# Performance work log

Measured on AMD Instinct MI355X. Metric: run time of the kernel, lower is better.

The kernel has to match this reference:

```python
import jax, jax.numpy as jnp
import numpy as np


def setup_inputs() -> dict:
    key = jax.random.key(0)
    ks = jax.random.split(key, 8)
    B, N, A, H = 2, 2048, 256, 8
    KD = A // H  # key_dim per head = 32
    VD = A // H  # value_dim per head = 32
    return {
        "q_data": jax.random.normal(ks[0], (B, N, A), dtype=jnp.float32),
        "bias": jax.random.normal(ks[1], (B, N), dtype=jnp.float32),
        "nonbatched_bias": jax.random.normal(ks[2], (H, N, N), dtype=jnp.float32),
        "query_w": jax.random.normal(ks[3], (A, H, KD), dtype=jnp.float32) * 0.05,
        "query_b": jax.random.normal(ks[4], (1, H, KD), dtype=jnp.float32) * 0.05,
        "key_w": jax.random.normal(ks[5], (A, H, KD), dtype=jnp.float32) * 0.05,
        "value_w": jax.random.normal(ks[6], (A, H, VD), dtype=jnp.float32) * 0.05,
        "gating_w": jax.random.normal(ks[7], (A, H, VD), dtype=jnp.float32) * 0.05,
    }


def reference(q_data, bias, nonbatched_bias, query_w, query_b, key_w, value_w, gating_w):
    # q_data: [b, n, a]; bias: [b, n_k]; nonbatched_bias: [h, n_q, n_k]
    key_dim = query_w.shape[-1]
    scale = key_dim ** (-0.5)
    # projections (fused QKV in the original kernel)
    q = (jnp.einsum("bqa,ahc->bqhc", q_data, query_w) + query_b) * scale  # [b,q,h,c]
    k = jnp.einsum("bka,ahc->bkhc", q_data, key_w)                        # [b,k,h,c]
    v = jnp.einsum("bka,ahv->bkhv", q_data, value_w)                      # [b,k,h,v]
    # attention logits + batched bias (over keys) + shared nonbatched bias
    logits = jnp.einsum("bqhc,bkhc->bhqk", q, k)
    logits = logits + bias[:, None, None, :] + nonbatched_bias[None]
    weights = jax.nn.softmax(logits, axis=-1)                             # [b,h,q,k]
    weighted = jnp.einsum("bhqk,bkhv->bqhv", weights, v)                  # [b,q,h,v]
    # sigmoid gating branch fused after value projection
    gate = jax.nn.sigmoid(jnp.einsum("bqa,ahv->bqhv", q_data, gating_w))
    return weighted * gate                                                # [b,q,h,v]
```

## Files before the change

### kernel.cpp

```cpp
#include <hip/hip_runtime.h>
#include <stdint.h>

#define NTOK 2048
#define SCALE 0.17677669529663687f
#define SM_SHIFT 24.0f

typedef short s16x8 __attribute__((ext_vector_type(8)));
typedef unsigned short u16x8 __attribute__((ext_vector_type(8)));
typedef float f32x4 __attribute__((ext_vector_type(4)));

__device__ __forceinline__ unsigned short f2bf(float f) {
  unsigned int u = __builtin_bit_cast(unsigned int, f);
  u += 0x7fffu + ((u >> 16) & 1u);
  return (unsigned short)(u >> 16);
}

__device__ __forceinline__ void gld_lds16(const float* g, float* l) {
  __builtin_amdgcn_global_load_lds(
      (const __attribute__((address_space(1))) unsigned int*)g,
      (__attribute__((address_space(3))) unsigned int*)l, 16, 0, 0);
}

__global__ __launch_bounds__(256) void prep_weights_k(
    const float* __restrict__ qw, const float* __restrict__ kw,
    const float* __restrict__ vw, const float* __restrict__ gw,
    unsigned short* __restrict__ Wt) {
  __shared__ float tile[64][68];
  const int p = blockIdx.z;
  const int a0 = blockIdx.x * 64;
  const int n0 = blockIdx.y * 64;
  const float* src = (p == 0) ? qw : (p == 1) ? kw : (p == 2) ? vw : gw;
  const int tx = threadIdx.x & 15;
  const int ty = threadIdx.x >> 4;
#pragma unroll
  for (int kk = 0; kk < 4; kk++) {
    int ar = ty + kk * 16;
    float4 v = *reinterpret_cast<const float4*>(src + (a0 + ar) * 256 + n0 + tx * 4);
    tile[ar][tx * 4 + 0] = v.x; tile[ar][tx * 4 + 1] = v.y;
    tile[ar][tx * 4 + 2] = v.z; tile[ar][tx * 4 + 3] = v.w;
  }
  __syncthreads();
  unsigned short* dst = Wt + p * 65536;
#pragma unroll
  for (int kk = 0; kk < 4; kk++) {
    int nr = ty + kk * 16;
    ushort4 o;
    o.x = f2bf(tile[tx * 4 + 0][nr]);
    o.y = f2bf(tile[tx * 4 + 1][nr]);
    o.z = f2bf(tile[tx * 4 + 2][nr]);
    o.w = f2bf(tile[tx * 4 + 3][nr]);
    *reinterpret_cast<ushort4*>(dst + (n0 + nr) * 256 + a0 + tx * 4) = o;
  }
}

__global__ __launch_bounds__(256) void proj_k(
    const float* __restrict__ x, const unsigned short* __restrict__ Wt,
    const float* __restrict__ query_b,
    unsigned short* __restrict__ Qg, unsigned short* __restrict__ Kg,
    unsigned short* __restrict__ Vt, float* __restrict__ gate) {
  const int w = threadIdx.x >> 6;
  const int lane = threadIdx.x & 63;
  const int l15 = lane & 15;
  const int quad = lane >> 4;
  const int p = blockIdx.y >> 1;
  const int half = blockIdx.y & 1;
  const int rbase = blockIdx.x * 128 + w * 32;
  const unsigned short* wp = Wt + p * 65536;

  f32x4 acc[2][8];
#pragma unroll
  for (int rt = 0; rt < 2; rt++)
#pragma unroll
    for (int ct = 0; ct < 8; ct++) acc[rt][ct] = (f32x4){0.f, 0.f, 0.f, 0.f};

  for (int ks = 0; ks < 8; ks++) {
    const int kb = ks * 32;
    s16x8 af[2];
#pragma unroll
    for (int rt = 0; rt < 2; rt++) {
      const float* xr = x + (rbase + rt * 16 + l15) * 256 + kb + quad * 8;
      float4 f0 = *reinterpret_cast<const float4*>(xr);
      float4 f1 = *reinterpret_cast<const float4*>(xr + 4);
      u16x8 t;
      t[0] = f2bf(f0.x); t[1] = f2bf(f0.y); t[2] = f2bf(f0.z); t[3] = f2bf(f0.w);
      t[4] = f2bf(f1.x); t[5] = f2bf(f1.y); t[6] = f2bf(f1.z); t[7] = f2bf(f1.w);
      af[rt] = __builtin_bit_cast(s16x8, t);
    }
#pragma unroll
    for (int ct = 0; ct < 8; ct++) {
      uint4 bv = *reinterpret_cast<const uint4*>(
          wp + (half * 128 + ct * 16 + l15) * 256 + kb + quad * 8);
      s16x8 bfr = __builtin_bit_cast(s16x8, bv);
#pragma unroll
      for (int rt = 0; rt < 2; rt++)
        acc[rt][ct] = __builtin_amdgcn_mfma_f32_16x16x32_bf16(af[rt], bfr, acc[rt][ct], 0, 0, 0);
    }
  }

#pragma unroll
  for (int ct = 0; ct < 8; ct++) {
    const int cgl = half * 128 + ct * 16 + l15;
    const int h = cgl >> 5, c = cgl & 31;
#pragma unroll
    for (int rt = 0; rt < 2; rt++) {
      const int n0r = rbase + rt * 16 + quad * 4;
      const int bidx = n0r >> 11;
      const int nl0 = n0r & 2047;
      if (p == 0) {
        const float qb = query_b[cgl];
#pragma unroll
        for (int i = 0; i < 4; i++) {
          float v = (acc[rt][ct][i] + qb) * SCALE;
          Qg[(size_t)((bidx * 8 + h) * 2048 + nl0 + i) * 32 + c] = f2bf(v);
        }
      } else if (p == 1) {
#pragma unroll
        for (int i = 0; i < 4; i++)
          Kg[(size_t)((bidx * 8 + h) * 2048 + nl0 + i) * 32 + c] = f2bf(acc[rt][ct][i]);
      } else if (p == 2) {
        ushort4 o;
        o.x = f2bf(acc[rt][ct][0]); o.y = f2bf(acc[rt][ct][1]);
        o.z = f2bf(acc[rt][ct][2]); o.w = f2bf(acc[rt][ct][3]);
        *reinterpret_cast<ushort4*>(Vt + (size_t)((bidx * 8 + h) * 32 + c) * 2048 + nl0) = o;
      } else {
#pragma unroll
        for (int i = 0; i < 4; i++) {
          float s = 1.f / (1.f + __expf(-acc[rt][ct][i]));
          gate[(size_t)(bidx * 2048 + nl0 + i) * 256 + cgl] = s;
        }
      }
    }
  }
}

#define PST 72
__global__ __launch_bounds__(256, 4) void attn_k(
    const unsigned short* __restrict__ Qg, const unsigned short* __restrict__ Kg,
    const unsigned short* __restrict__ Vt, const float* __restrict__ bias,
    const float* __restrict__ nb,
    float* __restrict__ po, float* __restrict__ pl) {
  __shared__ float NbS[2][32 * 64];
  __shared__ unsigned short Ps[4 * 16 * PST];
  const int w = threadIdx.x >> 6;
  const int lane = threadIdx.x & 63;
  const int l15 = lane & 15;
  const int quad = lane >> 4;
  const int qsub = w >> 1;
  const int b = w & 1;
  const int h = blockIdx.y;
  const int sp = blockIdx.z;
  const int bh = b * 8 + h;
  const int qtile = blockIdx.x * 32;
  const int qbase = qtile + qsub * 16;
  const int kt0 = sp * 16;
  const unsigned short* Qp = Qg + (size_t)bh * 2048 * 32;
  const unsigned short* Kp = Kg + (size_t)bh * 2048 * 32;
  const unsigned short* Vp = Vt + (size_t)bh * 32 * 2048;
  const float* biasp = bias + b * 2048;
  unsigned short* Pw = Ps + w * 16 * PST;

  const float* nbl[2];
  {
    const float* nbt = nb + (size_t)h * 2048 * 2048 + (size_t)qtile * 2048;
#pragma unroll
    for (int j = 0; j < 2; j++) {
      const int r = w * 8 + j * 4 + (lane >> 4);
      const int cblk = (lane & 15) ^ (r & 7);
      nbl[j] = nbt + (size_t)r * 2048 + cblk * 4;
    }
  }

  s16x8 aq = __builtin_bit_cast(s16x8, *reinterpret_cast<const uint4*>(
      Qp + (size_t)(qbase + l15) * 32 + quad * 8));
  const int qr0 = qbase + quad * 4;

  int nbrow[4], nbkey[4];
#pragma unroll
  for (int i = 0; i < 4; i++) {
    const int rl = qsub * 16 + quad * 4 + i;
    nbrow[i] = rl * 64;
    nbkey[i] = rl & 7;
  }

  float lst[4];
  f32x4 o[2];
#pragma unroll
  for (int i = 0; i < 4; i++) lst[i] = 0.f;
#pragma unroll
  for (int vt = 0; vt < 2; vt++) o[vt] = (f32x4){0.f, 0.f, 0.f, 0.f};

  float bb[4];
#pragma unroll
  for (int ct = 0; ct < 4; ct++) bb[ct] = biasp[kt0 * 64 + ct * 16 + l15];

#pragma unroll
  for (int j = 0; j < 2; j++)
    gld_lds16(nbl[j] + kt0 * 64, &NbS[0][(w * 8 + j * 4) * 64]);
  __syncthreads();

#pragma unroll 2
  for (int kt = kt0; kt < kt0 + 16; kt++) {
    const int kb = kt * 64;
    const int cur = kt & 1, nxt = cur ^ 1;

    s16x8 bk[4];
#pragma unroll
    for (int ct = 0; ct < 4; ct++)
      bk[ct] = __builtin_bit_cast(s16x8, *reinterpret_cast<const uint4*>(
          Kp + (size_t)(kb + ct * 16 + l15) * 32 + quad * 8));

    s16x8 vbf[2][2];
#pragma unroll
    for (int kc = 0; kc < 2; kc++)
#pragma unroll
      for (int vt = 0; vt < 2; vt++)
        vbf[kc][vt] = __builtin_bit_cast(s16x8, *reinterpret_cast<const uint4*>(
            Vp + (size_t)(vt * 16 + l15) * 2048 + kb + kc * 32 + quad * 8));

    if (kt < kt0 + 15) {
#pragma unroll
      for (int j = 0; j < 2; j++)
        gld_lds16(nbl[j] + (kb + 64), &NbS[nxt][(w * 8 + j * 4) * 64]);
    }

    f32x4 s[4];
#pragma unroll
    for (int ct = 0; ct < 4; ct++) {
#pragma unroll
      for (int i = 0; i < 4; i++) {
        const int slot = ((ct * 4 + (l15 >> 2)) ^ nbkey[i]) * 4 + (l15 & 3);
        s[ct][i] = bb[ct] + NbS[cur][nbrow[i] + slot];
      }
    }

#pragma unroll
    for (int ct = 0; ct < 4; ct++)
      s[ct] = __builtin_amdgcn_mfma_f32_16x16x32_bf16(aq, bk[ct], s[ct], 0, 0, 0);

    if (kt < kt0 + 15) {
      const int kb2 = kb + 64;
#pragma unroll
      for (int ct = 0; ct < 4; ct++) bb[ct] = biasp[kb2 + ct * 16 + l15];
    }

#pragma unroll
    for (int i = 0; i < 4; i++) {
      float sum = 0.f;
#pragma unroll
      for (int ct = 0; ct < 4; ct++) {
        float pv = __expf(s[ct][i] - SM_SHIFT);
        Pw[(quad * 4 + i) * PST + ct * 16 + l15] = f2bf(pv);
        sum += pv;
      }
      lst[i] += sum;
    }

#pragma unroll
    for (int kc = 0; kc < 2; kc++) {
      s16x8 ap = __builtin_bit_cast(s16x8, *reinterpret_cast<const uint4*>(
          &Pw[l15 * PST + kc * 32 + quad * 8]));
#pragma unroll
      for (int vt = 0; vt < 2; vt++)
        o[vt] = __builtin_amdgcn_mfma_f32_16x16x32_bf16(ap, vbf[kc][vt], o[vt], 0, 0, 0);
    }

    __syncthreads();
  }

  const size_t pbase = (size_t)(sp * 16 + bh) * 2048;
#pragma unroll
  for (int vt = 0; vt < 2; vt++)
#pragma unroll
    for (int i = 0; i < 4; i++)
      po[(pbase + qr0 + i) * 32 + vt * 16 + l15] = o[vt][i];
#pragma unroll
  for (int i = 0; i < 4; i++) {
    lst[i] += __shfl_xor(lst[i], 1);
    lst[i] += __shfl_xor(lst[i], 2);
    lst[i] += __shfl_xor(lst[i], 4);
    lst[i] += __shfl_xor(lst[i], 8);
  }
  if (l15 == 0) {
#pragma unroll
    for (int i = 0; i < 4; i++) pl[pbase + qr0 + i] = lst[i];
  }
}

__global__ __launch_bounds__(256) void combine_k(
    const float* __restrict__ po, const float* __restrict__ pl,
    const float* __restrict__ gate, float* __restrict__ out) {
  const int bq = blockIdx.x;
  const int b = bq >> 11, q = bq & 2047;
  const int h = threadIdx.x >> 5, v = threadIdx.x & 31;
  const int bh = b * 8 + h;
  const size_t i0 = (size_t)(0 * 16 + bh) * 2048 + q;
  const size_t i1 = (size_t)(1 * 16 + bh) * 2048 + q;
  const float l = pl[i0] + pl[i1];
  const float ov = po[i0 * 32 + v] + po[i1 * 32 + v];
  const size_t oidx = (size_t)(b * 2048 + q) * 256 + h * 32 + v;
  out[oidx] = (ov / l) * gate[oidx];
}

extern "C" void kernel_launch(void* const* d_in, const int* in_sizes, int n_in,
                              void* d_out, int out_size, void* d_ws, size_t ws_size,
                              hipStream_t stream) {
  const float* q_data = (const float*)d_in[0];
  const float* bias = (const float*)d_in[1];
  const float* nbb = (const float*)d_in[2];
  const float* qw = (const float*)d_in[3];
  const float* qb = (const float*)d_in[4];
  const float* kw = (const float*)d_in[5];
  const float* vw = (const float*)d_in[6];
  const float* gw = (const float*)d_in[7];
  float* out = (float*)d_out;

  char* ws = (char*)d_ws;
  unsigned short* Wt = (unsigned short*)(ws + 0);
  unsigned short* Qg = (unsigned short*)(ws + 524288);
  unsigned short* Kg = (unsigned short*)(ws + 2621440);
  unsigned short* Vt = (unsigned short*)(ws + 4718592);
  float* gate = (float*)(ws + 6815744);
  float* po = (float*)(ws + 11010048);
  float* pl = (float*)(ws + 19398656);

  prep_weights_k<<<dim3(4, 4, 4), 256, 0, stream>>>(qw, kw, vw, gw, Wt);
  proj_k<<<dim3(32, 8), 256, 0, stream>>>(q_data, Wt, qb, Qg, Kg, Vt, gate);
  attn_k<<<dim3(64, 8, 2), 256, 0, stream>>>(Qg, Kg, Vt, bias, nbb, po, pl);
  combine_k<<<dim3(4096), 256, 0, stream>>>(po, pl, gate, out);
}
```

Before: 253.6 us.

## Bulk-load 512-key nonbatched-bias slab into LDS, split keys four ways with atomics

The attention kernel now loads each block's whole 32x512 slice of the nonbatched bias into a 64 KB LDS buffer up front. This removes the per-iteration double-buffered loads and the __syncthreads inside the key loop. K and V fragments are register double-buffered one tile ahead, and the key split grows from two to four blocks. Partial outputs and row sums are combined with atomicAdd into zeroed buffers (a memset is added), replacing the separate combine pass over two partial copies. The larger LDS footprint lowers occupancy (launch bounds drop to 2 blocks), and atomics add contention and make summation order nondeterministic.

```diff
diff --git a/kernel.cpp b/kernel.cpp
--- a/kernel.cpp
+++ b/kernel.cpp
@@ -134,12 +134,12 @@
 }
 
 #define PST 72
-__global__ __launch_bounds__(256, 4) void attn_k(
+__global__ __launch_bounds__(256, 2) void attn_k(
     const unsigned short* __restrict__ Qg, const unsigned short* __restrict__ Kg,
     const unsigned short* __restrict__ Vt, const float* __restrict__ bias,
     const float* __restrict__ nb,
     float* __restrict__ po, float* __restrict__ pl) {
-  __shared__ float NbS[2][32 * 64];
+  __shared__ float NbS[32 * 512];
   __shared__ unsigned short Ps[4 * 16 * PST];
   const int w = threadIdx.x >> 6;
   const int lane = threadIdx.x & 63;
@@ -152,35 +152,54 @@
   const int bh = b * 8 + h;
   const int qtile = blockIdx.x * 32;
   const int qbase = qtile + qsub * 16;
-  const int kt0 = sp * 16;
+  const int k0 = sp * 512;
   const unsigned short* Qp = Qg + (size_t)bh * 2048 * 32;
   const unsigned short* Kp = Kg + (size_t)bh * 2048 * 32;
   const unsigned short* Vp = Vt + (size_t)bh * 32 * 2048;
-  const float* biasp = bias + b * 2048;
+  const float* biasp = bias + b * 2048 + k0;
   unsigned short* Pw = Ps + w * 16 * PST;
-
-  const float* nbl[2];
-  {
-    const float* nbt = nb + (size_t)h * 2048 * 2048 + (size_t)qtile * 2048;
-#pragma unroll
-    for (int j = 0; j < 2; j++) {
-      const int r = w * 8 + j * 4 + (lane >> 4);
-      const int cblk = (lane & 15) ^ (r & 7);
-      nbl[j] = nbt + (size_t)r * 2048 + cblk * 4;
-    }
-  }
 
   s16x8 aq = __builtin_bit_cast(s16x8, *reinterpret_cast<const uint4*>(
       Qp + (size_t)(qbase + l15) * 32 + quad * 8));
   const int qr0 = qbase + quad * 4;
 
+  float bb[4];
+#pragma unroll
+  for (int ct = 0; ct < 4; ct++) bb[ct] = biasp[ct * 16 + l15];
+
+  s16x8 bk[2][4], vb[2][4];
+#pragma unroll
+  for (int ct = 0; ct < 4; ct++)
+    bk[0][ct] = __builtin_bit_cast(s16x8, *reinterpret_cast<const uint4*>(
+        Kp + (size_t)(k0 + ct * 16 + l15) * 32 + quad * 8));
+#pragma unroll
+  for (int kc = 0; kc < 2; kc++)
+#pragma unroll
+    for (int vt = 0; vt < 2; vt++)
+      vb[0][kc * 2 + vt] = __builtin_bit_cast(s16x8, *reinterpret_cast<const uint4*>(
+          Vp + (size_t)(vt * 16 + l15) * 2048 + k0 + kc * 32 + quad * 8));
+
+  {
+    const float* nbt = nb + (size_t)h * 2048 * 2048 + (size_t)qtile * 2048 + k0;
+#pragma unroll
+    for (int c = 0; c < 2; c++)
+#pragma unroll
+      for (int jr = 0; jr < 8; jr++) {
+        const int r = w * 8 + jr;
+        const float* src = nbt + (size_t)r * 2048 + c * 256 + (lane ^ (r & 7)) * 4;
+        gld_lds16(src, &NbS[r * 512 + c * 256]);
+      }
+  }
+  __syncthreads();
+
   int nbrow[4], nbkey[4];
 #pragma unroll
   for (int i = 0; i < 4; i++) {
     const int rl = qsub * 16 + quad * 4 + i;
-    nbrow[i] = rl * 64;
+    nbrow[i] = rl * 512;
     nbkey[i] = rl & 7;
   }
+  const int cl = l15 >> 2, cs = l15 & 3;
 
   float lst[4];
   f32x4 o[2];
@@ -189,58 +208,42 @@
 #pragma unroll
   for (int vt = 0; vt < 2; vt++) o[vt] = (f32x4){0.f, 0.f, 0.f, 0.f};
 
-  float bb[4];
-#pragma unroll
-  for (int ct = 0; ct < 4; ct++) bb[ct] = biasp[kt0 * 64 + ct * 16 + l15];
-
-#pragma unroll
-  for (int j = 0; j < 2; j++)
-    gld_lds16(nbl[j] + kt0 * 64, &NbS[0][(w * 8 + j * 4) * 64]);
-  __syncthreads();
-
-#pragma unroll 2
-  for (int kt = kt0; kt < kt0 + 16; kt++) {
-    const int kb = kt * 64;
-    const int cur = kt & 1, nxt = cur ^ 1;
-
-    s16x8 bk[4];
+#pragma unroll
+  for (int tt = 0; tt < 8; tt++) {
+    const int cur = tt & 1, nxt = cur ^ 1;
+    const int kb = k0 + tt * 64;
+
+    if (tt < 7) {
+      const int kb2 = kb + 64;
+#pragma unroll
+      for (int ct = 0; ct < 4; ct++)
+        bk[nxt][ct] = __builtin_bit_cast(s16x8, *reinterpret_cast<const uint4*>(
+            Kp + (size_t)(kb2 + ct * 16 + l15) * 32 + quad * 8));
+#pragma unroll
+      for (int kc = 0; kc < 2; kc++)
+#pragma unroll
+        for (int vt = 0; vt < 2; vt++)
+          vb[nxt][kc * 2 + vt] = __builtin_bit_cast(s16x8, *reinterpret_cast<const uint4*>(
+              Vp + (size_t)(vt * 16 + l15) * 2048 + kb2 + kc * 32 + quad * 8));
+    }
+
+    f32x4 s[4];
+#pragma unroll
+    for (int ct = 0; ct < 4; ct++) {
+#pragma unroll
+      for (int i = 0; i < 4; i++) {
+        const int blk = (tt * 16 + ct * 4 + cl) ^ nbkey[i];
+        s[ct][i] = bb[ct] + NbS[nbrow[i] + blk * 4 + cs];
+      }
+    }
+
 #pragma unroll
     for (int ct = 0; ct < 4; ct++)
-      bk[ct] = __builtin_bit_cast(s16x8, *reinterpret_cast<const uint4*>(
-          Kp + (size_t)(kb + ct * 16 + l15) * 32 + quad * 8));
-
-    s16x8 vbf[2][2];
-#pragma unroll
-    for (int kc = 0; kc < 2; kc++)
-#pragma unroll
-      for (int vt = 0; vt < 2; vt++)
-        vbf[kc][vt] = __builtin_bit_cast(s16x8, *reinterpret_cast<const uint4*>(
-            Vp + (size_t)(vt * 16 + l15) * 2048 + kb + kc * 32 + quad * 8));
-
-    if (kt < kt0 + 15) {
-#pragma unroll
-      for (int j = 0; j < 2; j++)
-        gld_lds16(nbl[j] + (kb + 64), &NbS[nxt][(w * 8 + j * 4) * 64]);
-    }
-
-    f32x4 s[4];
-#pragma unroll
-    for (int ct = 0; ct < 4; ct++) {
-#pragma unroll
-      for (int i = 0; i < 4; i++) {
-        const int slot = ((ct * 4 + (l15 >> 2)) ^ nbkey[i]) * 4 + (l15 & 3);
-        s[ct][i] = bb[ct] + NbS[cur][nbrow[i] + slot];
-      }
-    }
-
-#pragma unroll
-    for (int ct = 0; ct < 4; ct++)
-      s[ct] = __builtin_amdgcn_mfma_f32_16x16x32_bf16(aq, bk[ct], s[ct], 0, 0, 0);
-
-    if (kt < kt0 + 15) {
-      const int kb2 = kb + 64;
-#pragma unroll
-      for (int ct = 0; ct < 4; ct++) bb[ct] = biasp[kb2 + ct * 16 + l15];
+      s[ct] = __builtin_amdgcn_mfma_f32_16x16x32_bf16(aq, bk[cur][ct], s[ct], 0, 0, 0);
+
+    if (tt < 7) {
+#pragma unroll
+      for (int ct = 0; ct < 4; ct++) bb[ct] = biasp[(tt + 1) * 64 + ct * 16 + l15];
     }
 
 #pragma unroll
@@ -261,18 +264,16 @@
           &Pw[l15 * PST + kc * 32 + quad * 8]));
 #pragma unroll
       for (int vt = 0; vt < 2; vt++)
-        o[vt] = __builtin_amdgcn_mfma_f32_16x16x32_bf16(ap, vbf[kc][vt], o[vt], 0, 0, 0);
-    }
-
-    __syncthreads();
-  }
-
-  const size_t pbase = (size_t)(sp * 16 + bh) * 2048;
+        o[vt] = __builtin_amdgcn_mfma_f32_16x16x32_bf16(ap, vb[cur][kc * 2 + vt], o[vt], 0, 0, 0);
+    }
+  }
+
+  float* pr = po + ((size_t)bh * 2048 + qr0) * 32;
 #pragma unroll
   for (int vt = 0; vt < 2; vt++)
 #pragma unroll
     for (int i = 0; i < 4; i++)
-      po[(pbase + qr0 + i) * 32 + vt * 16 + l15] = o[vt][i];
+      atomicAdd(&pr[i * 32 + vt * 16 + l15], o[vt][i]);
 #pragma unroll
   for (int i = 0; i < 4; i++) {
     lst[i] += __shfl_xor(lst[i], 1);
@@ -282,23 +283,21 @@
   }
   if (l15 == 0) {
 #pragma unroll
-    for (int i = 0; i < 4; i++) pl[pbase + qr0 + i] = lst[i];
-  }
-}
-
-__global__ __launch_bounds__(256) void combine_k(
+    for (int i = 0; i < 4; i++)
+      atomicAdd(&pl[(size_t)bh * 2048 + qr0 + i], lst[i]);
+  }
+}
+
+__global__ __launch_bounds__(256) void finalize_k(
     const float* __restrict__ po, const float* __restrict__ pl,
     const float* __restrict__ gate, float* __restrict__ out) {
   const int bq = blockIdx.x;
   const int b = bq >> 11, q = bq & 2047;
   const int h = threadIdx.x >> 5, v = threadIdx.x & 31;
   const int bh = b * 8 + h;
-  const size_t i0 = (size_t)(0 * 16 + bh) * 2048 + q;
-  const size_t i1 = (size_t)(1 * 16 + bh) * 2048 + q;
-  const float l = pl[i0] + pl[i1];
-  const float ov = po[i0 * 32 + v] + po[i1 * 32 + v];
+  const size_t pi = (size_t)bh * 2048 + q;
   const size_t oidx = (size_t)(b * 2048 + q) * 256 + h * 32 + v;
-  out[oidx] = (ov / l) * gate[oidx];
+  out[oidx] = (po[pi * 32 + v] / pl[pi]) * gate[oidx];
 }
 
 extern "C" void kernel_launch(void* const* d_in, const int* in_sizes, int n_in,
@@ -321,10 +320,11 @@
   unsigned short* Vt = (unsigned short*)(ws + 4718592);
   float* gate = (float*)(ws + 6815744);
   float* po = (float*)(ws + 11010048);
-  float* pl = (float*)(ws + 19398656);
-
+  float* pl = (float*)(ws + 15204352);
+
+  hipMemsetAsync(ws + 11010048, 0, 4325376, stream);
   prep_weights_k<<<dim3(4, 4, 4), 256, 0, stream>>>(qw, kw, vw, gw, Wt);
   proj_k<<<dim3(32, 8), 256, 0, stream>>>(q_data, Wt, qb, Qg, Kg, Vt, gate);
-  attn_k<<<dim3(64, 8, 2), 256, 0, stream>>>(Qg, Kg, Vt, bias, nbb, po, pl);
-  combine_k<<<dim3(4096), 256, 0, stream>>>(po, pl, gate, out);
-}
+  attn_k<<<dim3(64, 8, 4), 256, 0, stream>>>(Qg, Kg, Vt, bias, nbb, po, pl);
+  finalize_k<<<dim3(4096), 256, 0, stream>>>(po, pl, gate, out);
+}
```

New measurement: 269.0 us. +6.1%, slower.

## Compute transposed QK^T and pass P to PV MFMA via lane shuffles

Applied to the files above, without the earlier changes.

Swaps the MFMA operands so the score tile comes out transposed, with each lane holding four consecutive keys for one query row. This lets the nonbatched-bias and bias loads become vector f32x4 reads. The bf16 probabilities are then rearranged into the A-operand layout of the PV MFMA with register shuffles instead of a round trip through an LDS staging buffer. This removes the Ps shared array and its scalar stores and reloads, at the cost of eight ds_bpermute-style shuffles plus selects per k-chunk. The row-sum reduction also simplifies to two cross-quad shuffles.

```diff
diff --git a/kernel.cpp b/kernel.cpp
--- a/kernel.cpp
+++ b/kernel.cpp
@@ -133,14 +133,12 @@
   }
 }
 
-#define PST 72
 __global__ __launch_bounds__(256, 4) void attn_k(
     const unsigned short* __restrict__ Qg, const unsigned short* __restrict__ Kg,
     const unsigned short* __restrict__ Vt, const float* __restrict__ bias,
     const float* __restrict__ nb,
     float* __restrict__ po, float* __restrict__ pl) {
   __shared__ float NbS[2][32 * 64];
-  __shared__ unsigned short Ps[4 * 16 * PST];
   const int w = threadIdx.x >> 6;
   const int lane = threadIdx.x & 63;
   const int l15 = lane & 15;
@@ -157,7 +155,6 @@
   const unsigned short* Kp = Kg + (size_t)bh * 2048 * 32;
   const unsigned short* Vp = Vt + (size_t)bh * 32 * 2048;
   const float* biasp = bias + b * 2048;
-  unsigned short* Pw = Ps + w * 16 * PST;
 
   const float* nbl[2];
   {
@@ -172,31 +169,28 @@
 
   s16x8 aq = __builtin_bit_cast(s16x8, *reinterpret_cast<const uint4*>(
       Qp + (size_t)(qbase + l15) * 32 + quad * 8));
-  const int qr0 = qbase + quad * 4;
-
-  int nbrow[4], nbkey[4];
-#pragma unroll
-  for (int i = 0; i < 4; i++) {
-    const int rl = qsub * 16 + quad * 4 + i;
-    nbrow[i] = rl * 64;
-    nbkey[i] = rl & 7;
-  }
-
-  float lst[4];
+
+  const int nrow = qsub * 16 + l15;
+  const int rkey = nrow & 7;
+
+  float lst = 0.f;
   f32x4 o[2];
 #pragma unroll
-  for (int i = 0; i < 4; i++) lst[i] = 0.f;
-#pragma unroll
   for (int vt = 0; vt < 2; vt++) o[vt] = (f32x4){0.f, 0.f, 0.f, 0.f};
 
-  float bb[4];
-#pragma unroll
-  for (int ct = 0; ct < 4; ct++) bb[ct] = biasp[kt0 * 64 + ct * 16 + l15];
+  f32x4 bb4[4];
+#pragma unroll
+  for (int ct = 0; ct < 4; ct++)
+    bb4[ct] = *reinterpret_cast<const f32x4*>(biasp + kt0 * 64 + ct * 16 + quad * 4);
 
 #pragma unroll
   for (int j = 0; j < 2; j++)
     gld_lds16(nbl[j] + kt0 * 64, &NbS[0][(w * 8 + j * 4) * 64]);
   __syncthreads();
+
+  const int sA = l15 + (quad & 1) * 32;
+  const int sB = sA + 16;
+  const bool loq = quad < 2;
 
 #pragma unroll 2
   for (int kt = kt0; kt < kt0 + 16; kt++) {
@@ -226,39 +220,51 @@
     f32x4 s[4];
 #pragma unroll
     for (int ct = 0; ct < 4; ct++) {
-#pragma unroll
-      for (int i = 0; i < 4; i++) {
-        const int slot = ((ct * 4 + (l15 >> 2)) ^ nbkey[i]) * 4 + (l15 & 3);
-        s[ct][i] = bb[ct] + NbS[cur][nbrow[i] + slot];
-      }
+      const f32x4 nbv = *reinterpret_cast<const f32x4*>(
+          &NbS[cur][nrow * 64 + (((ct * 4 + quad) ^ rkey) << 2)]);
+      s[ct] = bb4[ct] + nbv;
     }
 
 #pragma unroll
     for (int ct = 0; ct < 4; ct++)
-      s[ct] = __builtin_amdgcn_mfma_f32_16x16x32_bf16(aq, bk[ct], s[ct], 0, 0, 0);
+      s[ct] = __builtin_amdgcn_mfma_f32_16x16x32_bf16(bk[ct], aq, s[ct], 0, 0, 0);
 
     if (kt < kt0 + 15) {
-      const int kb2 = kb + 64;
-#pragma unroll
-      for (int ct = 0; ct < 4; ct++) bb[ct] = biasp[kb2 + ct * 16 + l15];
-    }
-
-#pragma unroll
-    for (int i = 0; i < 4; i++) {
-      float sum = 0.f;
-#pragma unroll
-      for (int ct = 0; ct < 4; ct++) {
-        float pv = __expf(s[ct][i] - SM_SHIFT);
-        Pw[(quad * 4 + i) * PST + ct * 16 + l15] = f2bf(pv);
-        sum += pv;
-      }
-      lst[i] += sum;
+#pragma unroll
+      for (int ct = 0; ct < 4; ct++)
+        bb4[ct] = *reinterpret_cast<const f32x4*>(biasp + kb + 64 + ct * 16 + quad * 4);
+    }
+
+    unsigned pk[4][2];
+#pragma unroll
+    for (int ct = 0; ct < 4; ct++) {
+      const float p0 = __expf(s[ct][0] - SM_SHIFT);
+      const float p1 = __expf(s[ct][1] - SM_SHIFT);
+      const float p2 = __expf(s[ct][2] - SM_SHIFT);
+      const float p3 = __expf(s[ct][3] - SM_SHIFT);
+      lst += (p0 + p1) + (p2 + p3);
+      pk[ct][0] = (unsigned)f2bf(p0) | ((unsigned)f2bf(p1) << 16);
+      pk[ct][1] = (unsigned)f2bf(p2) | ((unsigned)f2bf(p3) << 16);
     }
 
 #pragma unroll
     for (int kc = 0; kc < 2; kc++) {
-      s16x8 ap = __builtin_bit_cast(s16x8, *reinterpret_cast<const uint4*>(
-          &Pw[l15 * PST + kc * 32 + quad * 8]));
+      const unsigned ca0 = pk[2 * kc][0], ca1 = pk[2 * kc][1];
+      const unsigned cb0 = pk[2 * kc + 1][0], cb1 = pk[2 * kc + 1][1];
+      const unsigned a0 = (unsigned)__shfl((int)ca0, sA);
+      const unsigned b0 = (unsigned)__shfl((int)cb0, sA);
+      const unsigned a1 = (unsigned)__shfl((int)ca1, sA);
+      const unsigned b1 = (unsigned)__shfl((int)cb1, sA);
+      const unsigned a2 = (unsigned)__shfl((int)ca0, sB);
+      const unsigned b2 = (unsigned)__shfl((int)cb0, sB);
+      const unsigned a3 = (unsigned)__shfl((int)ca1, sB);
+      const unsigned b3 = (unsigned)__shfl((int)cb1, sB);
+      uint4 au;
+      au.x = loq ? a0 : b0;
+      au.y = loq ? a1 : b1;
+      au.z = loq ? a2 : b2;
+      au.w = loq ? a3 : b3;
+      const s16x8 ap = __builtin_bit_cast(s16x8, au);
 #pragma unroll
       for (int vt = 0; vt < 2; vt++)
         o[vt] = __builtin_amdgcn_mfma_f32_16x16x32_bf16(ap, vbf[kc][vt], o[vt], 0, 0, 0);
@@ -268,22 +274,15 @@
   }
 
   const size_t pbase = (size_t)(sp * 16 + bh) * 2048;
+  const int qr0 = qbase + quad * 4;
 #pragma unroll
   for (int vt = 0; vt < 2; vt++)
 #pragma unroll
     for (int i = 0; i < 4; i++)
       po[(pbase + qr0 + i) * 32 + vt * 16 + l15] = o[vt][i];
-#pragma unroll
-  for (int i = 0; i < 4; i++) {
-    lst[i] += __shfl_xor(lst[i], 1);
-    lst[i] += __shfl_xor(lst[i], 2);
-    lst[i] += __shfl_xor(lst[i], 4);
-    lst[i] += __shfl_xor(lst[i], 8);
-  }
-  if (l15 == 0) {
-#pragma unroll
-    for (int i = 0; i < 4; i++) pl[pbase + qr0 + i] = lst[i];
-  }
+  lst += __shfl_xor(lst, 16);
+  lst += __shfl_xor(lst, 32);
+  if (quad == 0) pl[pbase + qbase + l15] = lst;
 }
 
 __global__ __launch_bounds__(256) void combine_k(
```

Result: no change. 256.5 us (+1.2%).
